# Optimization experiments

Hardware: AMD Instinct MI355X
Metric: run time of the kernel (lower is better)

The kernel has to match this reference:

```python
import jax, jax.numpy as jnp
import numpy as np

# ---- static dims (match TextMMadapter / Hydra(d_model=128, d_state=16, d_conv=7, expand=2)) ----
HID = 4096          # LLM hidden size
DM = 128            # adapter bottleneck / hydra d_model
DIN = 2 * DM        # d_inner = expand * d_model = 256
DST = 16            # d_state
HD = 64             # headdim (Mamba2/Hydra default)
NH = DIN // HD      # nheads = 4
DCONV = 7
CONV_DIM = DIN + 2 * DST            # 288
DIN_PROJ = 2 * DIN + 2 * DST + 2 * NH  # 552
SEQ, BATCH = 2048, 4


def setup_inputs() -> dict:
    key = jax.random.key(0)
    ks = jax.random.split(key, 12)
    rn = lambda k, shape, s=0.02: jax.random.normal(k, shape, jnp.float32) * s
    dt = jnp.exp(jax.random.uniform(ks[5], (NH,), jnp.float32, np.log(1e-3), np.log(1e-1)))
    return dict(
        x=jax.random.normal(ks[0], (SEQ, BATCH, HID), jnp.float32),
        w_down=rn(ks[1], (DM, HID)), b_down=jnp.zeros((DM,), jnp.float32),
        w_up=rn(ks[2], (HID, DM)), b_up=jnp.zeros((HID,), jnp.float32),
        gate1=jnp.asarray(0.6, jnp.float32),
        hy_in_w=rn(ks[3], (DIN_PROJ, DM)),
        hy_conv_w=rn(ks[4], (CONV_DIM, 1, DCONV), 0.2),
        hy_conv_b=jnp.zeros((CONV_DIM,), jnp.float32),
        hy_dt_bias=jnp.log(jnp.expm1(dt)),               # inverse softplus of dt init
        hy_A_log=jnp.log(jax.random.uniform(ks[6], (NH,), jnp.float32, 1.0, 16.0)),
        hy_D=jnp.ones((NH,), jnp.float32),
        hy_fcD_w=rn(ks[7], (NH, DIN)),
        hy_norm_w=jnp.ones((DIN,), jnp.float32),
        hy_out_w=rn(ks[8], (DM, DIN)),
    )


def _causal_conv(x, w, b):
    # depthwise causal conv1d; x: (b,l,c), w: (c,1,k)
    y = jax.lax.conv_general_dilated(
        jnp.transpose(x, (0, 2, 1)), w, (1,), [(DCONV - 1, 0)],
        feature_group_count=CONV_DIM, dimension_numbers=("NCH", "OIH", "NCH"))
    return jnp.transpose(y, (0, 2, 1)) + b


def _ssm_scan(x, dt, A, B, C):
    # selective scan: h_t = exp(dt_t A) h_{t-1} + dt_t B_t x_t ; y_t = C_t . h_t
    # x:(b,l,h,p) dt:(b,l,h) A:(h,) B,C:(b,l,n)
    dA = jnp.exp(dt * A)            # (b,l,h)
    dBx = dt[..., None] * x         # (b,l,h,p)

    def step(h, t):
        dA_t, dBx_t, B_t, C_t = t
        h = dA_t[:, :, None, None] * h + dBx_t[..., None] * B_t[:, None, None, :]
        y = jnp.einsum("bhpn,bn->bhp", h, C_t)
        return h, y

    h0 = jnp.zeros((x.shape[0], NH, HD, DST), x.dtype)
    _, ys = jax.lax.scan(step, h0, (jnp.moveaxis(dA, 1, 0), jnp.moveaxis(dBx, 1, 0),
                                    jnp.moveaxis(B, 1, 0), jnp.moveaxis(C, 1, 0)))
    return jnp.moveaxis(ys, 0, 1)   # (b,l,h,p)


def _hydra(u, in_w, conv_w, conv_b, dt_bias, A_log, D, fcD_w, norm_w, out_w):
    b, l, _ = u.shape
    zxbcdt = u @ in_w.T                                   # (b,l,552)
    z = zxbcdt[..., :DIN]
    xBC = zxbcdt[..., DIN:DIN + CONV_DIM]
    dt2 = zxbcdt[..., DIN + CONV_DIM:]
    dt_fw = jax.nn.softplus(dt2[..., :NH] + dt_bias)
    dt_bw = jax.nn.softplus(jnp.flip(dt2[..., NH:], 1) + dt_bias)
    xBC = jax.nn.silu(_causal_conv(xBC, conv_w, conv_b))
    xs = xBC[..., :DIN]
    Bm = xBC[..., DIN:DIN + DST]
    Cm = xBC[..., DIN + DST:]
    A = -jnp.exp(A_log)
    x4 = xs.reshape(b, l, NH, HD)
    y_fw = _ssm_scan(x4, dt_fw, A, Bm, Cm).reshape(b, l, DIN)
    y_bw = jnp.flip(_ssm_scan(jnp.flip(x4, 1), dt_bw, A, jnp.flip(Bm, 1), jnp.flip(Cm, 1)).reshape(b, l, DIN), 1)
    zero = jnp.zeros((b, 1, DIN), u.dtype)
    # quasiseparable mixer: strictly-causal fw + strictly-anticausal bw + data-dependent diagonal
    y = jnp.concatenate([zero, y_fw[:, :-1]], 1) + jnp.concatenate([y_bw[:, 1:], zero], 1)
    y = y + xs * jnp.repeat(xs @ fcD_w.T + D, HD, axis=-1)
    yz = y * jax.nn.silu(z)                               # gated RMSNorm (norm after gate)
    y = yz * jax.lax.rsqrt(jnp.mean(jnp.square(yz), -1, keepdims=True) + 1e-5) * norm_w
    return y @ out_w.T


def reference(x, w_down, b_down, w_up, b_up, gate1, hy_in_w, hy_conv_w, hy_conv_b,
              hy_dt_bias, hy_A_log, hy_D, hy_fcD_w, hy_norm_w, hy_out_w):
    x_init = x                                            # (S,B,HID)
    h = x @ w_down.T + b_down                             # (S,B,128)
    h = jnp.transpose(h, (1, 0, 2))                       # (B,S,128)
    h = jax.nn.gelu(h, approximate=False)
    xmid = h
    hp = (hy_in_w, hy_conv_w, hy_conv_b, hy_dt_bias, hy_A_log, hy_D, hy_fcD_w, hy_norm_w, hy_out_w)
    h = _hydra(h, *hp)
    h = _hydra(h, *hp)
    alpha = jax.nn.sigmoid(gate1)
    h = alpha * xmid + (1.0 - alpha) * h
    h = xmid + h
    h = h @ w_up.T + b_up                                 # (B,S,HID)
    return x_init + jnp.transpose(h, (1, 0, 2))
```

## Files before the change

### kernel.cpp

```cpp
#include <hip/hip_runtime.h>
#include <hip/hip_bf16.h>
#include <math.h>

#define SEQL 2048
#define NB   4
#define HID  4096
#define DM   128
#define DIN  256
#define DST  16
#define HD   64
#define NH   4
#define CONV_DIM 288
#define DPROJ 552
#define MROWS (SEQL*NB)
#define TCH 64
#define NCHUNK (SEQL/TCH)
#define KSPLIT 4

typedef __attribute__((ext_vector_type(8))) short short8;
typedef __attribute__((ext_vector_type(4))) float f32x4;

__device__ __forceinline__ float siluf(float v){ return v / (1.f + expf(-v)); }
__device__ __forceinline__ float geluf(float v){ return 0.5f*v*(1.f + erff(v*0.70710678118654752f)); }
__device__ __forceinline__ float wave_sum(float v){
    #pragma unroll
    for (int o = 32; o > 0; o >>= 1) v += __shfl_xor(v, o, 64);
    return v;
}
__device__ __forceinline__ unsigned bfpack2(float a, float b){
    __hip_bfloat162 v = __float22bfloat162_rn(make_float2(a, b));
    return *reinterpret_cast<unsigned*>(&v);
}

__global__ __launch_bounds__(256) void k_prep_w(const float* __restrict__ w_down,
    const float* __restrict__ w_up, const float* __restrict__ in_w,
    const float* __restrict__ out_w,
    __hip_bfloat16* __restrict__ wd, __hip_bfloat16* __restrict__ wu,
    __hip_bfloat16* __restrict__ wi, __hip_bfloat16* __restrict__ wo)
{
    int idx = blockIdx.x*256 + threadIdx.x;
    if (idx < 524288) { wd[idx] = __float2bfloat16(w_down[idx]); return; }
    idx -= 524288;
    if (idx < 524288) { wu[idx] = __float2bfloat16(w_up[idx]); return; }
    idx -= 524288;
    if (idx < 71680) { wi[idx] = (idx < 552*128) ? __float2bfloat16(in_w[idx]) : __float2bfloat16(0.f); return; }
    idx -= 71680;
    if (idx < 32768) { wo[idx] = __float2bfloat16(out_w[idx]); }
}

__global__ __launch_bounds__(256) void k_down_mfma(const float* __restrict__ x,
    const __hip_bfloat16* __restrict__ wbf, float* __restrict__ partial)
{
    __shared__ __align__(16) short Abuf[64][72];
    __shared__ __align__(16) short Wbuf[128][72];
    const int tid = threadIdx.x;
    const int m0 = blockIdx.x * 64;
    const int ks = blockIdx.y;
    const int b  = m0 >> 11, l0 = m0 & 2047;
    const int lane = tid & 63, wv = tid >> 6;
    const int fr = lane & 15, q = lane >> 4;
    f32x4 acc[8];
    #pragma unroll
    for (int i = 0; i < 8; ++i) acc[i] = (f32x4){0.f,0.f,0.f,0.f};

    const int arow = tid >> 2, aseg = tid & 3;
    const int wrow = tid >> 1, wseg = tid & 1;

    const int kbase = ks * (HID/KSPLIT);
    for (int k0 = kbase; k0 < kbase + HID/KSPLIT; k0 += 64) {
        const float4* ap = (const float4*)(x + (size_t)((l0 + arow)*NB + b)*HID + k0 + aseg*16);
        float4 f0 = ap[0], f1 = ap[1], f2 = ap[2], f3 = ap[3];
        const uint4* wp = (const uint4*)(wbf + (size_t)wrow*HID + k0 + wseg*32);
        uint4 w0 = wp[0], w1 = wp[1], w2 = wp[2], w3 = wp[3];
        uint4 pk0, pk1;
        pk0.x = bfpack2(f0.x,f0.y); pk0.y = bfpack2(f0.z,f0.w);
        pk0.z = bfpack2(f1.x,f1.y); pk0.w = bfpack2(f1.z,f1.w);
        pk1.x = bfpack2(f2.x,f2.y); pk1.y = bfpack2(f2.z,f2.w);
        pk1.z = bfpack2(f3.x,f3.y); pk1.w = bfpack2(f3.z,f3.w);
        uint4* adst = (uint4*)&Abuf[arow][aseg*16];
        adst[0] = pk0; adst[1] = pk1;
        uint4* wdst = (uint4*)&Wbuf[wrow][wseg*32];
        wdst[0] = w0; wdst[1] = w1; wdst[2] = w2; wdst[3] = w3;
        __syncthreads();
        #pragma unroll
        for (int kh = 0; kh < 2; ++kh) {
            short8 af = *reinterpret_cast<const short8*>(&Abuf[wv*16 + fr][kh*32 + q*8]);
            #pragma unroll
            for (int ns = 0; ns < 8; ++ns) {
                short8 bf = *reinterpret_cast<const short8*>(&Wbuf[ns*16 + fr][kh*32 + q*8]);
                acc[ns] = __builtin_amdgcn_mfma_f32_16x16x32_bf16(af, bf, acc[ns], 0, 0, 0);
            }
        }
        __syncthreads();
    }
    #pragma unroll
    for (int ns = 0; ns < 8; ++ns)
        #pragma unroll
        for (int r = 0; r < 4; ++r)
            partial[((size_t)ks*MROWS + m0 + wv*16 + q*4 + r)*DM + ns*16 + fr] = acc[ns][r];
}

__global__ __launch_bounds__(256) void k_down_fix(const float* __restrict__ partial,
    const float* __restrict__ bias, float* __restrict__ xmid,
    __hip_bfloat16* __restrict__ ubf)
{
    size_t i4 = ((size_t)blockIdx.x*256 + threadIdx.x)*4;
    int n = (int)(i4 & (DM-1));
    float4 p0 = *(const float4*)&partial[i4];
    float4 p1 = *(const float4*)&partial[(size_t)MROWS*DM + i4];
    float4 p2 = *(const float4*)&partial[(size_t)2*MROWS*DM + i4];
    float4 p3 = *(const float4*)&partial[(size_t)3*MROWS*DM + i4];
    float4 bv = *(const float4*)&bias[n];
    float4 v;
    v.x = geluf(p0.x + p1.x + p2.x + p3.x + bv.x);
    v.y = geluf(p0.y + p1.y + p2.y + p3.y + bv.y);
    v.z = geluf(p0.z + p1.z + p2.z + p3.z + bv.z);
    v.w = geluf(p0.w + p1.w + p2.w + p3.w + bv.w);
    *(float4*)&xmid[i4] = v;
    uint2 pk; pk.x = bfpack2(v.x, v.y); pk.y = bfpack2(v.z, v.w);
    *(uint2*)&ubf[i4] = pk;
}

__global__ __launch_bounds__(256) void k_proj_in(const __hip_bfloat16* __restrict__ ubf,
    const __hip_bfloat16* __restrict__ wbf, float* __restrict__ zx)
{
    __shared__ __align__(16) short Abuf[64][136];
    __shared__ __align__(16) short Wbuf[80][136];
    const int tid = threadIdx.x;
    const int m0 = blockIdx.x*64;
    const int n0 = blockIdx.y*80;
    for (int i = tid; i < 64*16; i += 256) {
        int r = i >> 4, s = i & 15;
        *(uint4*)&Abuf[r][s*8] = *(const uint4*)&ubf[(size_t)(m0+r)*DM + s*8];
    }
    for (int i = tid; i < 80*16; i += 256) {
        int r = i >> 4, s = i & 15;
        *(uint4*)&Wbuf[r][s*8] = *(const uint4*)&wbf[(size_t)(n0+r)*DM + s*8];
    }
    __syncthreads();
    const int lane = tid & 63, wv = tid >> 6, fr = lane & 15, q = lane >> 4;
    f32x4 acc[5];
    #pragma unroll
    for (int i = 0; i < 5; ++i) acc[i] = (f32x4){0.f,0.f,0.f,0.f};
    #pragma unroll
    for (int kt = 0; kt < 4; ++kt) {
        short8 af = *reinterpret_cast<const short8*>(&Abuf[wv*16 + fr][kt*32 + q*8]);
        #pragma unroll
        for (int ns = 0; ns < 5; ++ns) {
            short8 bf = *reinterpret_cast<const short8*>(&Wbuf[ns*16 + fr][kt*32 + q*8]);
            acc[ns] = __builtin_amdgcn_mfma_f32_16x16x32_bf16(af, bf, acc[ns], 0, 0, 0);
        }
    }
    #pragma unroll
    for (int ns = 0; ns < 5; ++ns) {
        int n = n0 + ns*16 + fr;
        if (n < DPROJ) {
            #pragma unroll
            for (int r = 0; r < 4; ++r)
                zx[(size_t)(m0 + wv*16 + q*4 + r)*DPROJ + n] = acc[ns][r];
        }
    }
}

template<int PASS>
__global__ __launch_bounds__(256) void k_proj_out_t(const __hip_bfloat16* __restrict__ ynbf,
    const __hip_bfloat16* __restrict__ wbf, const float* __restrict__ xmid,
    const float* __restrict__ gate1,
    __hip_bfloat16* __restrict__ ubf, __hip_bfloat16* __restrict__ hcbf)
{
    __shared__ __align__(16) short Abuf[64][136];
    __shared__ __align__(16) short Wbuf[128][136];
    const int tid = threadIdx.x;
    const int m0 = blockIdx.x*64;
    const int lane = tid & 63, wv = tid >> 6, fr = lane & 15, q = lane >> 4;
    f32x4 acc[8];
    #pragma unroll
    for (int i = 0; i < 8; ++i) acc[i] = (f32x4){0.f,0.f,0.f,0.f};
    for (int kb = 0; kb < 2; ++kb) {
        if (kb) __syncthreads();
        for (int i = tid; i < 64*16; i += 256) {
            int r = i >> 4, s = i & 15;
            *(uint4*)&Abuf[r][s*8] = *(const uint4*)&ynbf[(size_t)(m0+r)*DIN + kb*128 + s*8];
        }
        for (int i = tid; i < 128*16; i += 256) {
            int r = i >> 4, s = i & 15;
            *(uint4*)&Wbuf[r][s*8] = *(const uint4*)&wbf[(size_t)r*DIN + kb*128 + s*8];
        }
        __syncthreads();
        #pragma unroll
        for (int kt = 0; kt < 4; ++kt) {
            short8 af = *reinterpret_cast<const short8*>(&Abuf[wv*16 + fr][kt*32 + q*8]);
            #pragma unroll
            for (int ns = 0; ns < 8; ++ns) {
                short8 bf = *reinterpret_cast<const short8*>(&Wbuf[ns*16 + fr][kt*32 + q*8]);
                acc[ns] = __builtin_amdgcn_mfma_f32_16x16x32_bf16(af, bf, acc[ns], 0, 0, 0);
            }
        }
    }
    float ca = 0.f, cb = 0.f;
    if (PASS == 1) {
        float al = 1.f / (1.f + expf(-gate1[0]));
        ca = 1.f + al; cb = 1.f - al;
    }
    #pragma unroll
    for (int ns = 0; ns < 8; ++ns)
        #pragma unroll
        for (int r = 0; r < 4; ++r) {
            int m = m0 + wv*16 + q*4 + r, n = ns*16 + fr;
            float v = acc[ns][r];
            if (PASS == 0) {
                ubf[(size_t)m*DM + n] = __float2bfloat16(v);
            } else {
                float xm = xmid[(size_t)m*DM + n];
                hcbf[(size_t)m*DM + n] = __float2bfloat16(ca*xm + cb*v);
            }
        }
}

__global__ __launch_bounds__(256) void k_up_mfma(const __hip_bfloat16* __restrict__ hc,
    const __hip_bfloat16* __restrict__ wbf, const float* __restrict__ b_up,
    const float* __restrict__ x, float* __restrict__ out)
{
    __shared__ __align__(16) short Abuf[64][136];
    __shared__ __align__(16) short Wbuf[128][136];
    const int tid = threadIdx.x;
    const int m0 = blockIdx.x*64;
    const int n0 = blockIdx.y*128;
    for (int i = tid; i < 64*16; i += 256) {
        int r = i >> 4, s = i & 15;
        *(uint4*)&Abuf[r][s*8] = *(const uint4*)&hc[(size_t)(m0+r)*DM + s*8];
    }
    for (int i = tid; i < 128*16; i += 256) {
        int r = i >> 4, s = i & 15;
        *(uint4*)&Wbuf[r][s*8] = *(const uint4*)&wbf[(size_t)(n0+r)*DM + s*8];
    }
    __syncthreads();
    const int lane = tid & 63, wv = tid >> 6, fr = lane & 15, q = lane >> 4;
    f32x4 acc[8];
    #pragma unroll
    for (int i = 0; i < 8; ++i) acc[i] = (f32x4){0.f,0.f,0.f,0.f};
    #pragma unroll
    for (int kt = 0; kt < 4; ++kt) {
        short8 af = *reinterpret_cast<const short8*>(&Abuf[wv*16 + fr][kt*32 + q*8]);
        #pragma unroll
        for (int ns = 0; ns < 8; ++ns) {
            short8 bf = *reinterpret_cast<const short8*>(&Wbuf[ns*16 + fr][kt*32 + q*8]);
            acc[ns] = __builtin_amdgcn_mfma_f32_16x16x32_bf16(af, bf, acc[ns], 0, 0, 0);
        }
    }
    #pragma unroll
    for (int r = 0; r < 4; ++r) {
        int m = m0 + wv*16 + q*4 + r;
        int b = m >> 11, l = m & 2047;
        size_t rowbase = (size_t)(l*NB + b)*HID + n0;
        #pragma unroll
        for (int ns = 0; ns < 8; ++ns) {
            int n = ns*16 + fr;
            out[rowbase + n] = acc[ns][r] + b_up[n0 + n] + x[rowbase + n];
        }
    }
}

__global__ __launch_bounds__(320) void k_conv(const float* __restrict__ zx,
    const float* __restrict__ cw, const float* __restrict__ cb,
    const float* __restrict__ dt_bias, const float* __restrict__ A_log,
    float* __restrict__ xBC, float* __restrict__ dtbuf, float* __restrict__ dAbuf)
{
    const int m = blockIdx.x;
    const int l = m & (SEQL-1), b = m >> 11;
    const int c = threadIdx.x;
    if (c < CONV_DIM) {
        float acc = cb[c];
        #pragma unroll
        for (int k = 0; k < 7; ++k) {
            int l2 = l - 6 + k;
            if (l2 >= 0)
                acc = fmaf(zx[(size_t)(b*SEQL + l2)*DPROJ + DIN + c], cw[c*7 + k], acc);
        }
        xBC[(size_t)m*CONV_DIM + c] = siluf(acc);
    } else if (c < CONV_DIM + 2*NH) {
        int j = c - CONV_DIM;
        int dir = j >> 2, hh = j & 3;
        float dtraw = zx[(size_t)(b*SEQL + l)*DPROJ + 544 + j] + dt_bias[hh];
        float dt = dtraw > 20.f ? dtraw : log1pf(expf(dtraw));
        float dA = expf(dt * (-expf(A_log[hh])));
        int pos = dir ? (SEQL-1 - l) : l;
        size_t o = (size_t)((dir*NH + hh)*NB + b)*SEQL + pos;
        dtbuf[o] = dt; dAbuf[o] = dA;
    }
}

__global__ __launch_bounds__(256) void k_scan_state(const float* __restrict__ xBC,
    const float* __restrict__ dtbuf, const float* __restrict__ dAbuf,
    float* __restrict__ Sbuf, float* __restrict__ Pbuf)
{
    const int bid = blockIdx.x;
    const int c   = bid & (NCHUNK-1);
    const int h   = (bid >> 5) & (NH-1);
    const int b   = (bid >> 7) & 3;
    const int dir = bid >> 9;
    const int tid = threadIdx.x;
    __shared__ float dA_s[TCH], dt_s[TCH];
    __shared__ float Xs[TCH][HD];
    __shared__ float Bs[TCH][DST];
    const size_t tb = (size_t)((dir*NH + h)*NB + b)*SEQL + c*TCH;
    if (tid < TCH) {
        dt_s[tid] = dtbuf[tb + tid];
        dA_s[tid] = dAbuf[tb + tid];
    }
    __syncthreads();
    #pragma unroll
    for (int t = 0; t < 4; ++t) {
        int idx = t*256 + tid;
        int k2 = idx >> 4, p4 = (idx & 15)*4;
        int l2 = dir ? (SEQL-1 - (c*TCH + k2)) : (c*TCH + k2);
        float4 v = *(const float4*)&xBC[(size_t)(b*SEQL + l2)*CONV_DIM + h*HD + p4];
        float sc = dt_s[k2];
        v.x *= sc; v.y *= sc; v.z *= sc; v.w *= sc;
        *(float4*)&Xs[k2][p4] = v;
    }
    {
        int k2 = tid >> 2, n4 = (tid & 3)*4;
        int l2 = dir ? (SEQL-1 - (c*TCH + k2)) : (c*TCH + k2);
        *(float4*)&Bs[k2][n4] = *(const float4*)&xBC[(size_t)(b*SEQL + l2)*CONV_DIM + DIN + n4];
    }
    __syncthreads();
    const int lane = tid & 63, w = tid >> 6;
    const int p = w*16 + (lane >> 2), ng = lane & 3;
    float s[4] = {0.f, 0.f, 0.f, 0.f};
    for (int k2 = 0; k2 < TCH; ++k2) {
        float dAv = dA_s[k2];
        float xa  = Xs[k2][p];
        float4 bv = *(const float4*)&Bs[k2][ng*4];
        s[0] = fmaf(dAv, s[0], xa*bv.x);
        s[1] = fmaf(dAv, s[1], xa*bv.y);
        s[2] = fmaf(dAv, s[2], xa*bv.z);
        s[3] = fmaf(dAv, s[3], xa*bv.w);
    }
    const size_t sb = (size_t)bid * 1024;
    float4 sv = {s[0], s[1], s[2], s[3]};
    *(float4*)&Sbuf[sb + (size_t)(p*16 + ng*4)] = sv;
    if (w == 0) {
        float pv = dA_s[lane];
        #pragma unroll
        for (int o = 32; o > 0; o >>= 1) pv *= __shfl_xor(pv, o, 64);
        if (lane == 0) Pbuf[bid] = pv;
    }
}

__global__ __launch_bounds__(64) void k_scan_combine2(const float* __restrict__ Sbuf,
    const float* __restrict__ Pbuf, float* __restrict__ Hbuf)
{
    const int gt = blockIdx.x*64 + threadIdx.x;
    const int g = gt >> 10, e = gt & 1023;
    float sv[NCHUNK], pw[NCHUNK];
    #pragma unroll
    for (int cc = 0; cc < NCHUNK; ++cc)
        sv[cc] = Sbuf[(size_t)(g*NCHUNK + cc)*1024 + e];
    #pragma unroll
    for (int cc = 0; cc < NCHUNK; ++cc)
        pw[cc] = Pbuf[g*NCHUNK + cc];
    float carry = 0.f;
    #pragma unroll
    for (int cc = 0; cc < NCHUNK; ++cc) {
        Hbuf[(size_t)(g*NCHUNK + cc)*1024 + e] = carry;
        carry = fmaf(pw[cc], carry, sv[cc]);
    }
}

__global__ __launch_bounds__(256) void k_scan_out(const float* __restrict__ xBC,
    const float* __restrict__ dtbuf, const float* __restrict__ dAbuf,
    const float* __restrict__ Hbuf, float* __restrict__ yfw, float* __restrict__ ybw)
{
    const int bid = blockIdx.x;
    const int c   = bid & (NCHUNK-1);
    const int h   = (bid >> 5) & (NH-1);
    const int b   = (bid >> 7) & 3;
    const int dir = bid >> 9;
    const int tid = threadIdx.x;
    __shared__ float dA_s[TCH], dt_s[TCH];
    __shared__ float Xs[TCH][HD];
    __shared__ float Bs[TCH][DST];
    __shared__ float Cs[TCH][DST];
    const size_t tb = (size_t)((dir*NH + h)*NB + b)*SEQL + c*TCH;
    if (tid < TCH) {
        dt_s[tid] = dtbuf[tb + tid];
        dA_s[tid] = dAbuf[tb + tid];
    }
    __syncthreads();
    #pragma unroll
    for (int t = 0; t < 4; ++t) {
        int idx = t*256 + tid;
        int k2 = idx >> 4, p4 = (idx & 15)*4;
        int l2 = dir ? (SEQL-1 - (c*TCH + k2)) : (c*TCH + k2);
        float4 v = *(const float4*)&xBC[(size_t)(b*SEQL + l2)*CONV_DIM + h*HD + p4];
        float sc = dt_s[k2];
        v.x *= sc; v.y *= sc; v.z *= sc; v.w *= sc;
        *(float4*)&Xs[k2][p4] = v;
    }
    {
        int k2 = tid >> 2, n4 = (tid & 3)*4;
        int l2 = dir ? (SEQL-1 - (c*TCH + k2)) : (c*TCH + k2);
        *(float4*)&Bs[k2][n4] = *(const float4*)&xBC[(size_t)(b*SEQL + l2)*CONV_DIM + DIN + n4];
        *(float4*)&Cs[k2][n4] = *(const float4*)&xBC[(size_t)(b*SEQL + l2)*CONV_DIM + DIN + DST + n4];
    }
    __syncthreads();
    const int lane = tid & 63, w = tid >> 6;
    const int p = w*16 + (lane >> 2), ng = lane & 3;
    const size_t hb = (size_t)bid * 1024;
    float4 hv = *(const float4*)&Hbuf[hb + (size_t)(p*16 + ng*4)];
    float s[4] = {hv.x, hv.y, hv.z, hv.w};
    float* yout = dir ? ybw : yfw;
    for (int k2 = 0; k2 < TCH; ++k2) {
        float dAv = dA_s[k2];
        float xa  = Xs[k2][p];
        float4 bv = *(const float4*)&Bs[k2][ng*4];
        float4 cv = *(const float4*)&Cs[k2][ng*4];
        s[0] = fmaf(dAv, s[0], xa*bv.x);
        s[1] = fmaf(dAv, s[1], xa*bv.y);
        s[2] = fmaf(dAv, s[2], xa*bv.z);
        s[3] = fmaf(dAv, s[3], xa*bv.w);
        float yp = s[0]*cv.x + s[1]*cv.y + s[2]*cv.z + s[3]*cv.w;
        yp += __shfl_xor(yp, 1, 64);
        yp += __shfl_xor(yp, 2, 64);
        if (ng == 0) {
            int l2 = dir ? (SEQL-1 - (c*TCH + k2)) : (c*TCH + k2);
            yout[(size_t)(b*SEQL + l2)*DIN + h*HD + p] = yp;
        }
    }
}

__global__ __launch_bounds__(256) void k_epi(const float* __restrict__ zx,
    const float* __restrict__ xBC, const float* __restrict__ yfw,
    const float* __restrict__ ybw, const float* __restrict__ fcD_w,
    const float* __restrict__ Dv, const float* __restrict__ norm_w,
    __hip_bfloat16* __restrict__ ynbf)
{
    const int m = blockIdx.x;
    const int l = m & (SEQL-1);
    const int d = threadIdx.x;
    const int lane = d & 63, wave = d >> 6;
    __shared__ float red[4][4];
    __shared__ float redq[4];
    float xs = xBC[(size_t)m*CONV_DIM + d];
    float yv = 0.f;
    if (l > 0)       yv += yfw[(size_t)(m-1)*DIN + d];
    if (l < SEQL-1)  yv += ybw[(size_t)(m+1)*DIN + d];
    float p0 = wave_sum(xs * fcD_w[0*DIN + d]);
    float p1 = wave_sum(xs * fcD_w[1*DIN + d]);
    float p2 = wave_sum(xs * fcD_w[2*DIN + d]);
    float p3 = wave_sum(xs * fcD_w[3*DIN + d]);
    if (lane == 0) { red[wave][0]=p0; red[wave][1]=p1; red[wave][2]=p2; red[wave][3]=p3; }
    __syncthreads();
    const int h = d >> 6;
    float scal = red[0][h] + red[1][h] + red[2][h] + red[3][h] + Dv[h];
    yv = fmaf(xs, scal, yv);
    float z  = zx[(size_t)m*DPROJ + d];
    float yz = yv * siluf(z);
    float q = wave_sum(yz*yz);
    if (lane == 0) redq[wave] = q;
    __syncthreads();
    float ms = (redq[0] + redq[1] + redq[2] + redq[3]) * (1.f/DIN);
    float r = rsqrtf(ms + 1e-5f);
    ynbf[(size_t)m*DIN + d] = __float2bfloat16(yz * r * norm_w[d]);
}

extern "C" void kernel_launch(void* const* d_in, const int* in_sizes, int n_in,
                              void* d_out, int out_size, void* d_ws, size_t ws_size,
                              hipStream_t stream)
{
    const float* x       = (const float*)d_in[0];
    const float* w_down  = (const float*)d_in[1];
    const float* b_down  = (const float*)d_in[2];
    const float* w_up    = (const float*)d_in[3];
    const float* b_up    = (const float*)d_in[4];
    const float* gate1   = (const float*)d_in[5];
    const float* in_w    = (const float*)d_in[6];
    const float* conv_w  = (const float*)d_in[7];
    const float* conv_b  = (const float*)d_in[8];
    const float* dt_bias = (const float*)d_in[9];
    const float* A_log   = (const float*)d_in[10];
    const float* Dv      = (const float*)d_in[11];
    const float* fcD_w   = (const float*)d_in[12];
    const float* norm_w  = (const float*)d_in[13];
    const float* out_w   = (const float*)d_in[14];
    float* out = (float*)d_out;
    float* ws  = (float*)d_ws;

    size_t off = 0;
    float* xmid = ws + off; off += (size_t)MROWS*DM;
    float* zx   = ws + off; off += (size_t)MROWS*DPROJ;
    float* xBC  = ws + off; off += (size_t)MROWS*CONV_DIM;
    float* yfw  = ws + off; off += (size_t)MROWS*DIN;
    float* ybw  = ws + off; off += (size_t)MROWS*DIN;
    float* Sbuf = ws + off; off += (size_t)1024*1024;
    float* Pbuf = ws + off; off += 1024;
    float* Hbuf = ws + off; off += (size_t)1024*1024;
    float* dtbuf= ws + off; off += (size_t)2*NH*NB*SEQL;
    float* dAbuf= ws + off; off += (size_t)2*NH*NB*SEQL;
    __hip_bfloat16* bfb = (__hip_bfloat16*)(ws + off);
    size_t bo = 0;
    __hip_bfloat16* wd_bf = bfb + bo; bo += 524288;
    __hip_bfloat16* wu_bf = bfb + bo; bo += 524288;
    __hip_bfloat16* wi_bf = bfb + bo; bo += 71680;
    __hip_bfloat16* wo_bf = bfb + bo; bo += 32768;
    __hip_bfloat16* u_bf  = bfb + bo; bo += (size_t)MROWS*DM;
    __hip_bfloat16* yn_bf = bfb + bo; bo += (size_t)MROWS*DIN;
    __hip_bfloat16* hc_bf = bfb + bo; bo += (size_t)MROWS*DM;
    float* partial = zx;

    k_prep_w<<<4504, 256, 0, stream>>>(w_down, w_up, in_w, out_w, wd_bf, wu_bf, wi_bf, wo_bf);

    dim3 gdown(MROWS/64, KSPLIT);
    k_down_mfma<<<gdown, 256, 0, stream>>>(x, wd_bf, partial);
    k_down_fix<<<MROWS*DM/1024, 256, 0, stream>>>(partial, b_down, xmid, u_bf);

    for (int pass = 0; pass < 2; ++pass) {
        dim3 gin(MROWS/64, 7);
        k_proj_in<<<gin, 256, 0, stream>>>(u_bf, wi_bf, zx);
        k_conv<<<MROWS, 320, 0, stream>>>(zx, conv_w, conv_b, dt_bias, A_log, xBC, dtbuf, dAbuf);
        k_scan_state<<<1024, 256, 0, stream>>>(xBC, dtbuf, dAbuf, Sbuf, Pbuf);
        k_scan_combine2<<<512, 64, 0, stream>>>(Sbuf, Pbuf, Hbuf);
        k_scan_out<<<1024, 256, 0, stream>>>(xBC, dtbuf, dAbuf, Hbuf, yfw, ybw);
        k_epi<<<MROWS, 256, 0, stream>>>(zx, xBC, yfw, ybw, fcD_w, Dv, norm_w, yn_bf);
        if (pass == 0)
            k_proj_out_t<0><<<MROWS/64, 256, 0, stream>>>(yn_bf, wo_bf, xmid, gate1, u_bf, hc_bf);
        else
            k_proj_out_t<1><<<MROWS/64, 256, 0, stream>>>(yn_bf, wo_bf, xmid, gate1, u_bf, hc_bf);
    }

    dim3 gup(MROWS/64, HID/128);
    k_up_mfma<<<gup, 256, 0, stream>>>(hc_bf, wu_bf, b_up, x, out);
}
```

Before: 503.9 us.

## Fuse chunk-carry combine into scan output kernel, dropping Hbuf round trip

Removes the separate chunk-combine kernel and its Hbuf buffer. Each scan-output block now recomputes its incoming carry state by serially folding all preceding chunk states from Sbuf, and that fold overlaps with the shared-memory staging before the barrier. This saves one launch and a 4 MB write and read. In exchange it adds redundant reads: a late chunk does up to 31 serial loads per thread, so total Sbuf traffic grows and later chunks take longer.

```diff
diff --git a/kernel.cpp b/kernel.cpp
--- a/kernel.cpp
+++ b/kernel.cpp
@@ -301,8 +301,8 @@
     const int dir = bid >> 9;
     const int tid = threadIdx.x;
     __shared__ float dA_s[TCH], dt_s[TCH];
-    __shared__ float Xs[TCH][HD];
-    __shared__ float Bs[TCH][DST];
+    __shared__ __align__(16) float Xs[TCH][HD];
+    __shared__ __align__(16) float Bs[TCH][DST];
     const size_t tb = (size_t)((dir*NH + h)*NB + b)*SEQL + c*TCH;
     if (tid < TCH) {
         dt_s[tid] = dtbuf[tb + tid];
@@ -348,51 +348,29 @@
     }
 }
 
-__global__ __launch_bounds__(64) void k_scan_combine2(const float* __restrict__ Sbuf,
-    const float* __restrict__ Pbuf, float* __restrict__ Hbuf)
-{
-    const int gt = blockIdx.x*64 + threadIdx.x;
-    const int g = gt >> 10, e = gt & 1023;
-    float sv[NCHUNK], pw[NCHUNK];
-    #pragma unroll
-    for (int cc = 0; cc < NCHUNK; ++cc)
-        sv[cc] = Sbuf[(size_t)(g*NCHUNK + cc)*1024 + e];
-    #pragma unroll
-    for (int cc = 0; cc < NCHUNK; ++cc)
-        pw[cc] = Pbuf[g*NCHUNK + cc];
-    float carry = 0.f;
-    #pragma unroll
-    for (int cc = 0; cc < NCHUNK; ++cc) {
-        Hbuf[(size_t)(g*NCHUNK + cc)*1024 + e] = carry;
-        carry = fmaf(pw[cc], carry, sv[cc]);
-    }
-}
-
-__global__ __launch_bounds__(256) void k_scan_out(const float* __restrict__ xBC,
+__global__ __launch_bounds__(256) void k_scan_out2(const float* __restrict__ xBC,
     const float* __restrict__ dtbuf, const float* __restrict__ dAbuf,
-    const float* __restrict__ Hbuf, float* __restrict__ yfw, float* __restrict__ ybw)
+    const float* __restrict__ Sbuf, const float* __restrict__ Pbuf,
+    float* __restrict__ yfw, float* __restrict__ ybw)
 {
     const int bid = blockIdx.x;
-    const int c   = bid & (NCHUNK-1);
+    const int cs  = bid & (NCHUNK-1);
     const int h   = (bid >> 5) & (NH-1);
     const int b   = (bid >> 7) & 3;
     const int dir = bid >> 9;
     const int tid = threadIdx.x;
     __shared__ float dA_s[TCH], dt_s[TCH];
-    __shared__ float Xs[TCH][HD];
-    __shared__ float Bs[TCH][DST];
-    __shared__ float Cs[TCH][DST];
-    const size_t tb = (size_t)((dir*NH + h)*NB + b)*SEQL + c*TCH;
-    if (tid < TCH) {
-        dt_s[tid] = dtbuf[tb + tid];
-        dA_s[tid] = dAbuf[tb + tid];
-    }
+    __shared__ __align__(16) float Xs[TCH][HD];
+    __shared__ __align__(16) float Bs[TCH][DST];
+    __shared__ __align__(16) float Cs[TCH][DST];
+    const size_t tb = (size_t)((dir*NH + h)*NB + b)*SEQL + cs*TCH;
+    if (tid < TCH) { dt_s[tid] = dtbuf[tb + tid]; dA_s[tid] = dAbuf[tb + tid]; }
     __syncthreads();
     #pragma unroll
     for (int t = 0; t < 4; ++t) {
         int idx = t*256 + tid;
         int k2 = idx >> 4, p4 = (idx & 15)*4;
-        int l2 = dir ? (SEQL-1 - (c*TCH + k2)) : (c*TCH + k2);
+        int l2 = dir ? (SEQL-1 - (cs*TCH + k2)) : (cs*TCH + k2);
         float4 v = *(const float4*)&xBC[(size_t)(b*SEQL + l2)*CONV_DIM + h*HD + p4];
         float sc = dt_s[k2];
         v.x *= sc; v.y *= sc; v.z *= sc; v.w *= sc;
@@ -400,31 +378,48 @@
     }
     {
         int k2 = tid >> 2, n4 = (tid & 3)*4;
-        int l2 = dir ? (SEQL-1 - (c*TCH + k2)) : (c*TCH + k2);
+        int l2 = dir ? (SEQL-1 - (cs*TCH + k2)) : (cs*TCH + k2);
         *(float4*)&Bs[k2][n4] = *(const float4*)&xBC[(size_t)(b*SEQL + l2)*CONV_DIM + DIN + n4];
         *(float4*)&Cs[k2][n4] = *(const float4*)&xBC[(size_t)(b*SEQL + l2)*CONV_DIM + DIN + DST + n4];
     }
-    __syncthreads();
     const int lane = tid & 63, w = tid >> 6;
     const int p = w*16 + (lane >> 2), ng = lane & 3;
-    const size_t hb = (size_t)bid * 1024;
-    float4 hv = *(const float4*)&Hbuf[hb + (size_t)(p*16 + ng*4)];
-    float s[4] = {hv.x, hv.y, hv.z, hv.w};
+    const float* Sg = Sbuf + (size_t)(bid - cs)*1024 + (p*16 + ng*4);
+    const float* Pg = Pbuf + (bid - cs);
+    float4 carry = {0.f,0.f,0.f,0.f};
+    for (int jb = 0; jb < cs; jb += 8) {
+        float4 sv[8]; float pw[8];
+        #pragma unroll
+        for (int k = 0; k < 8; ++k) {
+            int j = jb + k;
+            if (j < cs) { sv[k] = *(const float4*)(Sg + (size_t)j*1024); pw[k] = Pg[j]; }
+            else        { sv[k] = (float4){0.f,0.f,0.f,0.f}; pw[k] = 1.f; }
+        }
+        #pragma unroll
+        for (int k = 0; k < 8; ++k) {
+            carry.x = fmaf(pw[k], carry.x, sv[k].x);
+            carry.y = fmaf(pw[k], carry.y, sv[k].y);
+            carry.z = fmaf(pw[k], carry.z, sv[k].z);
+            carry.w = fmaf(pw[k], carry.w, sv[k].w);
+        }
+    }
+    __syncthreads();
+    float s0 = carry.x, s1 = carry.y, s2 = carry.z, s3 = carry.w;
     float* yout = dir ? ybw : yfw;
     for (int k2 = 0; k2 < TCH; ++k2) {
         float dAv = dA_s[k2];
         float xa  = Xs[k2][p];
         float4 bv = *(const float4*)&Bs[k2][ng*4];
         float4 cv = *(const float4*)&Cs[k2][ng*4];
-        s[0] = fmaf(dAv, s[0], xa*bv.x);
-        s[1] = fmaf(dAv, s[1], xa*bv.y);
-        s[2] = fmaf(dAv, s[2], xa*bv.z);
-        s[3] = fmaf(dAv, s[3], xa*bv.w);
-        float yp = s[0]*cv.x + s[1]*cv.y + s[2]*cv.z + s[3]*cv.w;
+        s0 = fmaf(dAv, s0, xa*bv.x);
+        s1 = fmaf(dAv, s1, xa*bv.y);
+        s2 = fmaf(dAv, s2, xa*bv.z);
+        s3 = fmaf(dAv, s3, xa*bv.w);
+        float yp = s0*cv.x + s1*cv.y + s2*cv.z + s3*cv.w;
         yp += __shfl_xor(yp, 1, 64);
         yp += __shfl_xor(yp, 2, 64);
         if (ng == 0) {
-            int l2 = dir ? (SEQL-1 - (c*TCH + k2)) : (c*TCH + k2);
+            int l2 = dir ? (SEQL-1 - (cs*TCH + k2)) : (cs*TCH + k2);
             yout[(size_t)(b*SEQL + l2)*DIN + h*HD + p] = yp;
         }
     }
@@ -495,7 +490,6 @@
     float* ybw  = ws + off; off += (size_t)MROWS*DIN;
     float* Sbuf = ws + off; off += (size_t)1024*1024;
     float* Pbuf = ws + off; off += 1024;
-    float* Hbuf = ws + off; off += (size_t)1024*1024;
     float* dtbuf= ws + off; off += (size_t)2*NH*NB*SEQL;
     float* dAbuf= ws + off; off += (size_t)2*NH*NB*SEQL;
     __hip_bfloat16* bfb = (__hip_bfloat16*)(ws + off);
@@ -520,8 +514,7 @@
         k_proj_in<<<gin, 256, 0, stream>>>(u_bf, wi_bf, zx);
         k_conv<<<MROWS, 320, 0, stream>>>(zx, conv_w, conv_b, dt_bias, A_log, xBC, dtbuf, dAbuf);
         k_scan_state<<<1024, 256, 0, stream>>>(xBC, dtbuf, dAbuf, Sbuf, Pbuf);
-        k_scan_combine2<<<512, 64, 0, stream>>>(Sbuf, Pbuf, Hbuf);
-        k_scan_out<<<1024, 256, 0, stream>>>(xBC, dtbuf, dAbuf, Hbuf, yfw, ybw);
+        k_scan_out2<<<1024, 256, 0, stream>>>(xBC, dtbuf, dAbuf, Sbuf, Pbuf, yfw, ybw);
         k_epi<<<MROWS, 256, 0, stream>>>(zx, xBC, yfw, ybw, fcD_w, Dv, norm_w, yn_bf);
         if (pass == 0)
             k_proj_out_t<0><<<MROWS/64, 256, 0, stream>>>(yn_bf, wo_bf, xmid, gate1, u_bf, hc_bf);
```

Result: no change. 501.3 us (-0.5%).
